# Optimization experiments

Measured on AMD Instinct MI355X. Metric: run time of the kernel, lower is better.

The kernel has to match this reference:

```python
import jax, jax.numpy as jnp
import numpy as np

EMBED = 200
ATT_D = 200
EPS = 1e-5


def _make_pos(x, embed_len):
    # p[i, j+off, k] = sin(j/1000^(j/E)) if k odd else cos(...); rows with leading
    # zero-count `off` get positions shifted right; first `off` rows stay zero.
    B, L = x.shape
    off = jnp.sum(x == 0, axis=1)                       # [B]
    j = jnp.arange(L)[None, :] - off[:, None]           # [B, L]
    valid = j >= 0
    jf = jnp.maximum(j, 0).astype(jnp.float32)
    angle = jf / jnp.power(1000.0, jf / embed_len)      # [B, L]
    kk = jnp.arange(embed_len)
    odd = (kk % 2 == 1)[None, None, :]
    val = jnp.where(odd, jnp.sin(angle)[:, :, None], jnp.cos(angle)[:, :, None])
    return jnp.where(valid[:, :, None], val, 0.0)       # [B, L, E]


def _ln2(y):
    # F.layer_norm over last TWO dims (seq, embed), no affine
    mu = jnp.mean(y, axis=(1, 2), keepdims=True)
    var = jnp.mean((y - mu) ** 2, axis=(1, 2), keepdims=True)
    return (y - mu) / jnp.sqrt(var + EPS)


def setup_inputs() -> dict:
    key = jax.random.key(0)
    ks = jax.random.split(key, 10)
    B, L, V = 32, 1024, 32000
    x = jax.random.randint(ks[0], (B, L), 0, V)
    embed = jax.random.normal(ks[1], (V, EMBED), dtype=jnp.float32) * 0.02
    w_qkv = jax.random.normal(ks[2], (EMBED, ATT_D), dtype=jnp.float32) * 0.02
    b_qkv = jnp.zeros((ATT_D,), dtype=jnp.float32)
    head = 8
    w_fuse = jax.random.normal(ks[3], (ATT_D * head, ATT_D), dtype=jnp.float32) * 0.02
    b_fuse = jnp.zeros((ATT_D,), dtype=jnp.float32)
    w1 = jax.random.normal(ks[4], (ATT_D, ATT_D), dtype=jnp.float32) * 0.02
    b1 = jnp.zeros((ATT_D,), dtype=jnp.float32)
    w2 = jax.random.normal(ks[5], (ATT_D, ATT_D), dtype=jnp.float32) * 0.02
    b2 = jnp.zeros((ATT_D,), dtype=jnp.float32)
    return {"x": x, "embed": embed, "w_qkv": w_qkv, "b_qkv": b_qkv,
            "w_fuse": w_fuse, "b_fuse": b_fuse, "w1": w1, "b1": b1,
            "w2": w2, "b2": b2, "stack": 6, "head": head}


def reference(x, embed, w_qkv, b_qkv, w_fuse, b_fuse, w1, b1, w2, b2, stack, head):
    p = _make_pos(x, EMBED)
    h = embed[x] + p                                     # [B, L, 200]
    scale = jnp.sqrt(jnp.float32(ATT_D))
    for _ in range(stack):
        r = h
        # q == k == v: the source shares ONE Linear across q/k/v, heads, stacks
        q = h @ w_qkv + b_qkv                            # [B, L, 200]
        d = jnp.einsum('bld,bmd->blm', q, q) / scale     # [B, L, L]
        a = jax.nn.softmax(d, axis=-1)
        c = jnp.einsum('blm,bmd->bld', a, q)             # [B, L, 200]
        c_all = jnp.tile(c, (1, 1, head))                # identical heads concat
        h = c_all @ w_fuse + b_fuse
        h = _ln2(h + r)
        r = h
        h = jax.nn.relu(h @ w1 + b1) @ w2 + b2
        h = _ln2(h + r)
    return h
```

## Files before the change

kernel.cpp:

```cpp
#include <hip/hip_runtime.h>
#include <hip/hip_bf16.h>

#define B_    32
#define L_    1024
#define D_    200
#define DP    256
#define M_    (B_*L_)
#define NTOT  (M_*DP)
#define NELEM 204800.f
#define INVSCALE 0.07071067811865475f
#define LNEPS 1e-5f

typedef unsigned short u16;
typedef unsigned int   u32;
typedef long long      i64;
typedef __attribute__((ext_vector_type(8))) short bf16x8;
typedef __attribute__((ext_vector_type(4))) float f32x4;

__device__ __forceinline__ float bf2f(u32 lo16) {
    union { u32 i; float f; } v; v.i = lo16 << 16; return v.f;
}
__device__ __forceinline__ u16 f2bf(float f) {
    union { float f; u32 i; } v; v.f = f;
    u32 r = v.i + 0x7fffu + ((v.i >> 16) & 1u);
    return (u16)(r >> 16);
}
__device__ __forceinline__ float ldf(const void* p, long i, int isbf) {
    return isbf ? bf2f(((const u16*)p)[i]) : ((const float*)p)[i];
}
__device__ __forceinline__ i64 ldtok(const void* p, long i, int isl64) {
    return isl64 ? ((const i64*)p)[i] : (i64)((const int*)p)[i];
}

__global__ void k_dtype(const u16* __restrict__ e16, const u32* __restrict__ xw,
                        int* __restrict__ flag) {
    int t = threadIdx.x;
    u32 u = e16[2*t];
    u32 ex = (u >> 7) & 0xFFu;
    int sane = (ex >= 0x60u && ex <= 0x87u) ? 1 : 0;
    unsigned long long m1 = __ballot(sane);
    int zhi = (xw[2*t + 1] == 0u) ? 1 : 0;
    unsigned long long m2 = __ballot(zhi);
    if (t == 0) {
        flag[0] = (__popcll(m1) >= 48) ? 1 : 0;
        flag[1] = (__popcll(m2) >= 48) ? 1 : 0;
    }
}

__global__ void k_off(const void* __restrict__ x, const int* __restrict__ flag,
                      int* __restrict__ off) {
    __shared__ int red[256];
    int b = blockIdx.x, t = threadIdx.x;
    int isl64 = flag[1];
    int cnt = 0;
    for (int l = t; l < L_; l += 256)
        cnt += (ldtok(x, (long)b*L_ + l, isl64) == 0) ? 1 : 0;
    red[t] = cnt; __syncthreads();
    for (int s = 128; s > 0; s >>= 1) {
        if (t < s) red[t] += red[t+s];
        __syncthreads();
    }
    if (t == 0) off[b] = red[0];
}

__global__ void k_wfold(const void* __restrict__ wqkv,
                        const void* __restrict__ wfuse,
                        const void* __restrict__ w1,
                        const void* __restrict__ w2,
                        const int* __restrict__ flag,
                        u16* __restrict__ tq, u16* __restrict__ tf,
                        u16* __restrict__ t1, u16* __restrict__ t2) {
    int idx = blockIdx.x*256 + threadIdx.x;
    if (idx >= DP*DP) return;
    int isbf = flag[0];
    int n = idx / DP, k = idx % DP;
    float vq = 0.f, vf = 0.f, v1 = 0.f, v2 = 0.f;
    if (n < D_ && k < D_) {
        vq = ldf(wqkv, k*D_ + n, isbf);
        v1 = ldf(w1,   k*D_ + n, isbf);
        v2 = ldf(w2,   k*D_ + n, isbf);
        #pragma unroll
        for (int hh = 0; hh < 8; ++hh)
            vf += ldf(wfuse, (hh*D_ + k)*D_ + n, isbf);
    }
    tq[idx] = f2bf(vq); tf[idx] = f2bf(vf);
    t1[idx] = f2bf(v1); t2[idx] = f2bf(v2);
}

__global__ void k_bfold(const void* __restrict__ bqkv, const void* __restrict__ bfuse,
                        const void* __restrict__ b1,   const void* __restrict__ b2,
                        const int* __restrict__ flag,
                        float* __restrict__ pq, float* __restrict__ pf,
                        float* __restrict__ p1, float* __restrict__ p2,
                        float* __restrict__ part, float* __restrict__ statA) {
    int c = threadIdx.x;
    int isbf = flag[0];
    float vq = 0.f, vf = 0.f, v1 = 0.f, v2 = 0.f;
    if (c < D_) {
        vq = ldf(bqkv, c, isbf); vf = ldf(bfuse, c, isbf);
        v1 = ldf(b1,   c, isbf); v2 = ldf(b2,   c, isbf);
    }
    pq[c] = vq; pf[c] = vf; p1[c] = v1; p2[c] = v2;
    if (c < 64) part[c] = 0.f;
    if (c < 32) { statA[2*c] = 0.f; statA[2*c+1] = 1.f; }
}

__global__ void k_embed(const void* __restrict__ x,
                        const void* __restrict__ emb,
                        const int* __restrict__ off,
                        const int* __restrict__ flag,
                        float* __restrict__ A) {
    int idx = blockIdx.x*256 + threadIdx.x;
    int c = idx & 255;
    int l = (idx >> 8) & 1023;
    int b = idx >> 18;
    float v = 0.f;
    if (c < D_) {
        i64 tok = ldtok(x, (long)b*L_ + l, flag[1]);
        v = ldf(emb, (long)tok*D_ + c, flag[0]);
        int j = l - off[b];
        if (j >= 0) {
            float jf = (float)j;
            float angle = jf * __expf(-jf * 0.034538776394910684f);
            v += (c & 1) ? __sinf(angle) : __cosf(angle);
        }
    }
    A[idx] = v;
}

template<int ACT, int OBF, int RES, int LNA>
__global__ __launch_bounds__(256) void k_gemm_m(const void* __restrict__ Asrc,
                                                const u16* __restrict__ Wt,
                                                const float* __restrict__ biasp,
                                                void* __restrict__ C,
                                                const float* __restrict__ Res,
                                                const float* __restrict__ rstat,
                                                float* __restrict__ part) {
    __shared__ u16 wt3[32*1032];
    const int t    = threadIdx.x;
    const int lane = t & 63;
    const int w    = t >> 6;
    const int quad = lane >> 4;
    const int l16  = lane & 15;
    const int r0   = blockIdx.x * 128;
    const int c0   = blockIdx.y * 128;

    float mu = 0.f, inv = 1.f;
    if (LNA || RES) {
        int batch = blockIdx.x >> 3;
        mu  = rstat[2*batch];
        inv = rstat[2*batch + 1];
    }

    #pragma unroll
    for (int i = 0; i < 16; ++i) {
        int ci = t + i*256;
        int n = ci >> 5, kc = ci & 31;
        *(uint4*)&wt3[kc*1032 + n*8] =
            *(const uint4*)(Wt + (size_t)(c0 + n)*DP + kc*8);
    }

    bf16x8 qa[2][7];
    #pragma unroll
    for (int rb = 0; rb < 2; ++rb) {
        size_t ro = (size_t)(r0 + w*32 + rb*16 + l16)*DP + quad*8;
        if (LNA) {
            const float* ar = (const float*)Asrc + ro;
            #pragma unroll
            for (int kk = 0; kk < 7; ++kk) {
                f32x4 va = *(const f32x4*)(ar + kk*32);
                f32x4 vb = *(const f32x4*)(ar + kk*32 + 4);
                bf16x8 q;
                q[0] = (short)f2bf((va[0]-mu)*inv);
                q[1] = (short)f2bf((va[1]-mu)*inv);
                q[2] = (short)f2bf((va[2]-mu)*inv);
                q[3] = (short)f2bf((va[3]-mu)*inv);
                q[4] = (short)f2bf((vb[0]-mu)*inv);
                q[5] = (short)f2bf((vb[1]-mu)*inv);
                q[6] = (short)f2bf((vb[2]-mu)*inv);
                q[7] = (short)f2bf((vb[3]-mu)*inv);
                qa[rb][kk] = q;
            }
        } else {
            const u16* ar = (const u16*)Asrc + ro;
            #pragma unroll
            for (int kk = 0; kk < 7; ++kk)
                qa[rb][kk] = *(const bf16x8*)(ar + kk*32);
        }
    }
    __syncthreads();

    f32x4 acc[2][8];
    #pragma unroll
    for (int rb = 0; rb < 2; ++rb)
        #pragma unroll
        for (int ct = 0; ct < 8; ++ct) acc[rb][ct] = (f32x4){0.f,0.f,0.f,0.f};

    #pragma unroll
    for (int ct = 0; ct < 8; ++ct) {
        #pragma unroll
        for (int kk = 0; kk < 7; ++kk) {
            bf16x8 vb = *(const bf16x8*)&wt3[(kk*4 + quad)*1032 + (ct*16 + l16)*8];
            acc[0][ct] = __builtin_amdgcn_mfma_f32_16x16x32_bf16(qa[0][kk], vb, acc[0][ct], 0,0,0);
            acc[1][ct] = __builtin_amdgcn_mfma_f32_16x16x32_bf16(qa[1][kk], vb, acc[1][ct], 0,0,0);
        }
    }

    float lsum = 0.f, lss = 0.f;
    #pragma unroll
    for (int ct = 0; ct < 8; ++ct) {
        int col = c0 + ct*16 + l16;
        float bv = biasp[col];
        #pragma unroll
        for (int rb = 0; rb < 2; ++rb) {
            #pragma unroll
            for (int r = 0; r < 4; ++r) {
                int row = r0 + w*32 + rb*16 + quad*4 + r;
                float v = acc[rb][ct][r] + bv;
                if (ACT) v = fmaxf(v, 0.f);
                if (RES) {
                    v += (Res[(size_t)row*DP + col] - mu) * inv;
                    ((float*)C)[(size_t)row*DP + col] = v;
                    if (col < D_) { lsum += v; lss += v*v; }
                } else if (OBF) {
                    ((u16*)C)[(size_t)row*DP + col] = f2bf(v);
                } else {
                    ((float*)C)[(size_t)row*DP + col] = v;
                }
            }
        }
    }
    if (RES) {
        __syncthreads();
        float* red = (float*)wt3;
        red[t] = lsum; red[256 + t] = lss;
        __syncthreads();
        for (int s = 128; s > 0; s >>= 1) {
            if (t < s) { red[t] += red[t+s]; red[256+t] += red[256+t+s]; }
            __syncthreads();
        }
        if (t == 0) {
            int batch = blockIdx.x >> 3;
            atomicAdd(&part[2*batch],     red[0]);
            atomicAdd(&part[2*batch + 1], red[256]);
        }
    }
}

__global__ __launch_bounds__(256) void k_tr(const u16* __restrict__ Qbf,
                                            u16* __restrict__ QbfT) {
    __shared__ u16 tile[64][72];
    const int t  = threadIdx.x;
    const int k0 = blockIdx.x * 64;
    const int f0 = blockIdx.y * 64;
    const int b  = blockIdx.z;
    const u16* S = Qbf  + (size_t)b*(L_*DP);
    u16*      Dd = QbfT + (size_t)b*(L_*DP);
    #pragma unroll
    for (int i = 0; i < 2; ++i) {
        int ci = t + i*256;
        int row = ci >> 3, g = ci & 7;
        *(uint4*)&tile[row][g*8] =
            *(const uint4*)(S + (size_t)(k0+row)*DP + f0 + g*8);
    }
    __syncthreads();
    #pragma unroll
    for (int i = 0; i < 2; ++i) {
        int ci = t + i*256;
        int feat = ci >> 3, g = ci & 7;
        u16 tmp[8];
        #pragma unroll
        for (int e = 0; e < 8; ++e) tmp[e] = tile[g*8+e][feat];
        *(uint4*)(Dd + (size_t)(f0+feat)*L_ + k0 + g*8) = *(uint4*)tmp;
    }
}

__global__ __launch_bounds__(256) void k_attn_m(const u16* __restrict__ Qbf,
                                                const u16* __restrict__ QbfT,
                                                u16* __restrict__ O) {
    __shared__ u16 ks[32*264];
    __shared__ u16 vt[256*40];
    __shared__ u16 ps[64*40];
    const int t    = threadIdx.x;
    const int lane = t & 63;
    const int w    = t >> 6;
    const int quad = lane >> 4;
    const int l16  = lane & 15;
    const int id   = blockIdx.x;
    const int xcd  = id & 7;
    const int ti   = (id >> 3) & 15;
    const int b    = ((id >> 7) << 3) | xcd;
    const int l0   = ti * 64;
    const u16* Qb  = Qbf  + (size_t)b*(L_*DP);
    const u16* QTb = QbfT + (size_t)b*(L_*DP);
    u16*       Ob  = O    + (size_t)b*(L_*DP);

    bf16x8 qa[7];
    {
        const u16* qrow = Qb + (size_t)(l0 + w*16 + l16)*DP + quad*8;
        #pragma unroll
        for (int kk = 0; kk < 7; ++kk)
            qa[kk] = *(const bf16x8*)(qrow + kk*32);
    }
    f32x4 oacc[13];
    #pragma unroll
    for (int ft = 0; ft < 13; ++ft) oacc[ft] = (f32x4){0.f, 0.f, 0.f, 0.f};
    float l_acc[4] = {0.f, 0.f, 0.f, 0.f};

    for (int n0 = 0; n0 < L_; n0 += 32) {
        __syncthreads();
        #pragma unroll
        for (int i = 0; i < 4; ++i) {
            int ci = t + i*256;
            int row = ci >> 5, g = ci & 31;
            *(uint4*)&ks[row*264 + g*8] =
                *(const uint4*)(Qb + (size_t)(n0+row)*DP + g*8);
        }
        #pragma unroll
        for (int i = 0; i < 4; ++i) {
            int ci = t + i*256;
            int feat = ci >> 2, g = ci & 3;
            *(uint4*)&vt[feat*40 + g*8] =
                *(const uint4*)(QTb + (size_t)feat*L_ + n0 + g*8);
        }
        __syncthreads();
        #pragma unroll
        for (int ct = 0; ct < 2; ++ct) {
            f32x4 sc = (f32x4){0.f, 0.f, 0.f, 0.f};
            #pragma unroll
            for (int kk = 0; kk < 7; ++kk) {
                bf16x8 bb = *(const bf16x8*)&ks[(ct*16 + l16)*264 + kk*32 + quad*8];
                sc = __builtin_amdgcn_mfma_f32_16x16x32_bf16(qa[kk], bb, sc, 0, 0, 0);
            }
            #pragma unroll
            for (int r = 0; r < 4; ++r) {
                float p = __expf(sc[r] * INVSCALE);
                l_acc[r] += p;
                ps[(w*16 + quad*4 + r)*40 + ct*16 + l16] = f2bf(p);
            }
        }
        __syncthreads();
        bf16x8 pa = *(const bf16x8*)&ps[(w*16 + l16)*40 + quad*8];
        #pragma unroll
        for (int ft = 0; ft < 13; ++ft) {
            bf16x8 vb = *(const bf16x8*)&vt[(ft*16 + l16)*40 + quad*8];
            oacc[ft] = __builtin_amdgcn_mfma_f32_16x16x32_bf16(pa, vb, oacc[ft], 0, 0, 0);
        }
    }
    #pragma unroll
    for (int r = 0; r < 4; ++r) {
        float v = l_acc[r];
        v += __shfl_xor(v, 1);
        v += __shfl_xor(v, 2);
        v += __shfl_xor(v, 4);
        v += __shfl_xor(v, 8);
        l_acc[r] = 1.f / v;
    }
    #pragma unroll
    for (int r = 0; r < 4; ++r) {
        u16* orow = Ob + (size_t)(l0 + w*16 + quad*4 + r)*DP + l16;
        #pragma unroll
        for (int ft = 0; ft < 13; ++ft)
            orow[ft*16] = f2bf(oacc[ft][r] * l_acc[r]);
        orow[13*16] = 0; orow[14*16] = 0; orow[15*16] = 0;
    }
}

__global__ void k_ln_stats(float* __restrict__ part, float* __restrict__ stats) {
    int b = threadIdx.x;
    if (b >= 32) return;
    float sum = part[2*b], ss = part[2*b+1];
    float mu  = sum / NELEM;
    float var = ss / NELEM - mu*mu;
    stats[b*2]   = mu;
    stats[b*2+1] = 1.f / sqrtf(var + LNEPS);
    part[2*b] = 0.f; part[2*b+1] = 0.f;
}

__global__ void k_out(const float* __restrict__ A, const float* __restrict__ stat,
                      const int* __restrict__ flag, float* __restrict__ out) {
    int idx = blockIdx.x*256 + threadIdx.x;
    if (idx >= M_*D_) return;
    int row = idx / D_;
    int c   = idx - row*D_;
    int b   = row >> 10;
    float v = (A[(size_t)row*DP + c] - stat[2*b]) * stat[2*b+1];
    if (!isfinite(v)) v = 1000.f + 64.f*flag[0] + 16.f*flag[1];
    out[idx] = v;
}

extern "C" void kernel_launch(void* const* d_in, const int* in_sizes, int n_in,
                              void* d_out, int out_size, void* d_ws, size_t ws_size,
                              hipStream_t stream) {
    const void* x     = d_in[0];
    const void* emb   = d_in[1];
    const void* wqkv  = d_in[2];
    const void* bqkv  = d_in[3];
    const void* wfuse = d_in[4];
    const void* bfuse = d_in[5];
    const void* w1    = d_in[6];
    const void* b1    = d_in[7];
    const void* w2    = d_in[8];
    const void* b2    = d_in[9];

    float* Y0  = (float*)d_ws;
    float* Y1  = Y0 + NTOT;
    u16* Qbf   = (u16*)(Y1 + NTOT);
    u16* QbfT  = Qbf + NTOT;
    u16* Hbf   = QbfT;
    u16* Cbf   = QbfT + NTOT;
    u16* wtq   = Cbf + NTOT;
    u16* wtf   = wtq + DP*DP;
    u16* wt1   = wtf + DP*DP;
    u16* wt2   = wt1 + DP*DP;
    float* bqp = (float*)(wt2 + DP*DP);
    float* bfp = bqp + DP;
    float* b1p = bfp + DP;
    float* b2p = b1p + DP;
    float* part  = b2p + DP;
    float* statA = part + 64;
    float* statB = statA + 64;
    int*   off   = (int*)(statB + 64);
    int*   flag  = off + 32;

    k_dtype<<<1, 64, 0, stream>>>((const u16*)emb, (const u32*)x, flag);
    k_off  <<<32, 256, 0, stream>>>(x, flag, off);
    k_wfold<<<DP*DP/256, 256, 0, stream>>>(wqkv, wfuse, w1, w2, flag,
                                           wtq, wtf, wt1, wt2);
    k_bfold<<<1, 256, 0, stream>>>(bqkv, bfuse, b1, b2, flag,
                                   bqp, bfp, b1p, b2p, part, statA);
    k_embed<<<NTOT/256, 256, 0, stream>>>(x, emb, off, flag, Y0);

    for (int s = 0; s < 6; ++s) {
        k_gemm_m<0,1,0,1><<<dim3(M_/128, DP/128), 256, 0, stream>>>(
            Y0, wtq, bqp, Qbf, nullptr, statA, nullptr);
        k_tr<<<dim3(L_/64, DP/64, B_), 256, 0, stream>>>(Qbf, QbfT);
        k_attn_m<<<512, 256, 0, stream>>>(Qbf, QbfT, Cbf);
        k_gemm_m<0,0,1,0><<<dim3(M_/128, DP/128), 256, 0, stream>>>(
            Cbf, wtf, bfp, Y1, Y0, statA, part);
        k_ln_stats<<<1, 64, 0, stream>>>(part, statB);
        k_gemm_m<1,1,0,1><<<dim3(M_/128, DP/128), 256, 0, stream>>>(
            Y1, wt1, b1p, Hbf, nullptr, statB, nullptr);
        k_gemm_m<0,0,1,0><<<dim3(M_/128, DP/128), 256, 0, stream>>>(
            Hbf, wt2, b2p, Y0, Y1, statB, part);
        k_ln_stats<<<1, 64, 0, stream>>>(part, statA);
    }
    k_out<<<(M_*D_ + 255)/256, 256, 0, stream>>>(Y0, statA, flag, (float*)d_out);
}
```

Baseline: 984.9 us.

## Fuse Q transpose into QKV GEMM epilogue and widen attention per-wave row tiles

The QKV GEMM epilogue now also writes the transposed bf16 Q directly into QbfT using 8-byte strided stores, so the separate k_tr transpose kernel is gone. The attention kernel moves to 128-thread blocks in which each wave handles 32 query rows (two 16-row tiles). Each K/V fragment loaded from LDS is reused for two MFMAs, and the barrier before reading P is dropped because each wave reads back only the rows it wrote. The trade-offs are more registers per wave, half as many waves per block, and strided transposed global writes in the GEMM epilogue.

```diff
diff --git a/kernel.cpp b/kernel.cpp
--- a/kernel.cpp
+++ b/kernel.cpp
@@ -128,14 +128,15 @@
     A[idx] = v;
 }
 
-template<int ACT, int OBF, int RES, int LNA>
+template<int ACT, int OBF, int RES, int LNA, int TRW>
 __global__ __launch_bounds__(256) void k_gemm_m(const void* __restrict__ Asrc,
                                                 const u16* __restrict__ Wt,
                                                 const float* __restrict__ biasp,
                                                 void* __restrict__ C,
                                                 const float* __restrict__ Res,
                                                 const float* __restrict__ rstat,
-                                                float* __restrict__ part) {
+                                                float* __restrict__ part,
+                                                u16* __restrict__ Qt) {
     __shared__ u16 wt3[32*1032];
     const int t    = threadIdx.x;
     const int lane = t & 63;
@@ -213,6 +214,7 @@
         float bv = biasp[col];
         #pragma unroll
         for (int rb = 0; rb < 2; ++rb) {
+            u16 tq4[4];
             #pragma unroll
             for (int r = 0; r < 4; ++r) {
                 int row = r0 + w*32 + rb*16 + quad*4 + r;
@@ -223,10 +225,18 @@
                     ((float*)C)[(size_t)row*DP + col] = v;
                     if (col < D_) { lsum += v; lss += v*v; }
                 } else if (OBF) {
-                    ((u16*)C)[(size_t)row*DP + col] = f2bf(v);
+                    u16 hb = f2bf(v);
+                    ((u16*)C)[(size_t)row*DP + col] = hb;
+                    if (TRW) tq4[r] = hb;
                 } else {
                     ((float*)C)[(size_t)row*DP + col] = v;
                 }
+            }
+            if (TRW && OBF) {
+                size_t batch = (size_t)(r0 >> 10);
+                int key = (r0 & 1023) + w*32 + rb*16 + quad*4;
+                *(uint2*)(Qt + batch*(size_t)(DP*L_) + (size_t)col*L_ + key)
+                    = *(const uint2*)tq4;
             }
         }
     }
@@ -247,37 +257,9 @@
     }
 }
 
-__global__ __launch_bounds__(256) void k_tr(const u16* __restrict__ Qbf,
-                                            u16* __restrict__ QbfT) {
-    __shared__ u16 tile[64][72];
-    const int t  = threadIdx.x;
-    const int k0 = blockIdx.x * 64;
-    const int f0 = blockIdx.y * 64;
-    const int b  = blockIdx.z;
-    const u16* S = Qbf  + (size_t)b*(L_*DP);
-    u16*      Dd = QbfT + (size_t)b*(L_*DP);
-    #pragma unroll
-    for (int i = 0; i < 2; ++i) {
-        int ci = t + i*256;
-        int row = ci >> 3, g = ci & 7;
-        *(uint4*)&tile[row][g*8] =
-            *(const uint4*)(S + (size_t)(k0+row)*DP + f0 + g*8);
-    }
-    __syncthreads();
-    #pragma unroll
-    for (int i = 0; i < 2; ++i) {
-        int ci = t + i*256;
-        int feat = ci >> 3, g = ci & 7;
-        u16 tmp[8];
-        #pragma unroll
-        for (int e = 0; e < 8; ++e) tmp[e] = tile[g*8+e][feat];
-        *(uint4*)(Dd + (size_t)(f0+feat)*L_ + k0 + g*8) = *(uint4*)tmp;
-    }
-}
-
-__global__ __launch_bounds__(256) void k_attn_m(const u16* __restrict__ Qbf,
-                                                const u16* __restrict__ QbfT,
-                                                u16* __restrict__ O) {
+__global__ __launch_bounds__(128, 1) void k_attn_m(const u16* __restrict__ Qbf,
+                                                   const u16* __restrict__ QbfT,
+                                                   u16* __restrict__ O) {
     __shared__ u16 ks[32*264];
     __shared__ u16 vt[256*40];
     __shared__ u16 ps[64*40];
@@ -295,30 +277,33 @@
     const u16* QTb = QbfT + (size_t)b*(L_*DP);
     u16*       Ob  = O    + (size_t)b*(L_*DP);
 
-    bf16x8 qa[7];
-    {
-        const u16* qrow = Qb + (size_t)(l0 + w*16 + l16)*DP + quad*8;
+    bf16x8 qa[2][7];
+    #pragma unroll
+    for (int rb = 0; rb < 2; ++rb) {
+        const u16* qrow = Qb + (size_t)(l0 + w*32 + rb*16 + l16)*DP + quad*8;
         #pragma unroll
         for (int kk = 0; kk < 7; ++kk)
-            qa[kk] = *(const bf16x8*)(qrow + kk*32);
-    }
-    f32x4 oacc[13];
-    #pragma unroll
-    for (int ft = 0; ft < 13; ++ft) oacc[ft] = (f32x4){0.f, 0.f, 0.f, 0.f};
-    float l_acc[4] = {0.f, 0.f, 0.f, 0.f};
+            qa[rb][kk] = *(const bf16x8*)(qrow + kk*32);
+    }
+    f32x4 oacc[2][13];
+    #pragma unroll
+    for (int rb = 0; rb < 2; ++rb)
+        #pragma unroll
+        for (int ft = 0; ft < 13; ++ft) oacc[rb][ft] = (f32x4){0.f, 0.f, 0.f, 0.f};
+    float l_acc[2][4] = {{0.f,0.f,0.f,0.f},{0.f,0.f,0.f,0.f}};
 
     for (int n0 = 0; n0 < L_; n0 += 32) {
         __syncthreads();
         #pragma unroll
-        for (int i = 0; i < 4; ++i) {
-            int ci = t + i*256;
+        for (int i = 0; i < 8; ++i) {
+            int ci = t + i*128;
             int row = ci >> 5, g = ci & 31;
             *(uint4*)&ks[row*264 + g*8] =
                 *(const uint4*)(Qb + (size_t)(n0+row)*DP + g*8);
         }
         #pragma unroll
-        for (int i = 0; i < 4; ++i) {
-            int ci = t + i*256;
+        for (int i = 0; i < 8; ++i) {
+            int ci = t + i*128;
             int feat = ci >> 2, g = ci & 3;
             *(uint4*)&vt[feat*40 + g*8] =
                 *(const uint4*)(QTb + (size_t)feat*L_ + n0 + g*8);
@@ -326,44 +311,54 @@
         __syncthreads();
         #pragma unroll
         for (int ct = 0; ct < 2; ++ct) {
-            f32x4 sc = (f32x4){0.f, 0.f, 0.f, 0.f};
+            f32x4 sc0 = (f32x4){0.f, 0.f, 0.f, 0.f};
+            f32x4 sc1 = (f32x4){0.f, 0.f, 0.f, 0.f};
             #pragma unroll
             for (int kk = 0; kk < 7; ++kk) {
                 bf16x8 bb = *(const bf16x8*)&ks[(ct*16 + l16)*264 + kk*32 + quad*8];
-                sc = __builtin_amdgcn_mfma_f32_16x16x32_bf16(qa[kk], bb, sc, 0, 0, 0);
+                sc0 = __builtin_amdgcn_mfma_f32_16x16x32_bf16(qa[0][kk], bb, sc0, 0, 0, 0);
+                sc1 = __builtin_amdgcn_mfma_f32_16x16x32_bf16(qa[1][kk], bb, sc1, 0, 0, 0);
             }
             #pragma unroll
             for (int r = 0; r < 4; ++r) {
-                float p = __expf(sc[r] * INVSCALE);
-                l_acc[r] += p;
-                ps[(w*16 + quad*4 + r)*40 + ct*16 + l16] = f2bf(p);
+                float p0 = __expf(sc0[r] * INVSCALE);
+                float p1 = __expf(sc1[r] * INVSCALE);
+                l_acc[0][r] += p0;
+                l_acc[1][r] += p1;
+                ps[(w*32 +      quad*4 + r)*40 + ct*16 + l16] = f2bf(p0);
+                ps[(w*32 + 16 + quad*4 + r)*40 + ct*16 + l16] = f2bf(p1);
             }
         }
-        __syncthreads();
-        bf16x8 pa = *(const bf16x8*)&ps[(w*16 + l16)*40 + quad*8];
+        bf16x8 pa0 = *(const bf16x8*)&ps[(w*32      + l16)*40 + quad*8];
+        bf16x8 pa1 = *(const bf16x8*)&ps[(w*32 + 16 + l16)*40 + quad*8];
         #pragma unroll
         for (int ft = 0; ft < 13; ++ft) {
             bf16x8 vb = *(const bf16x8*)&vt[(ft*16 + l16)*40 + quad*8];
-            oacc[ft] = __builtin_amdgcn_mfma_f32_16x16x32_bf16(pa, vb, oacc[ft], 0, 0, 0);
-        }
-    }
-    #pragma unroll
-    for (int r = 0; r < 4; ++r) {
-        float v = l_acc[r];
-        v += __shfl_xor(v, 1);
-        v += __shfl_xor(v, 2);
-        v += __shfl_xor(v, 4);
-        v += __shfl_xor(v, 8);
-        l_acc[r] = 1.f / v;
-    }
-    #pragma unroll
-    for (int r = 0; r < 4; ++r) {
-        u16* orow = Ob + (size_t)(l0 + w*16 + quad*4 + r)*DP + l16;
-        #pragma unroll
-        for (int ft = 0; ft < 13; ++ft)
-            orow[ft*16] = f2bf(oacc[ft][r] * l_acc[r]);
-        orow[13*16] = 0; orow[14*16] = 0; orow[15*16] = 0;
-    }
+            oacc[0][ft] = __builtin_amdgcn_mfma_f32_16x16x32_bf16(pa0, vb, oacc[0][ft], 0, 0, 0);
+            oacc[1][ft] = __builtin_amdgcn_mfma_f32_16x16x32_bf16(pa1, vb, oacc[1][ft], 0, 0, 0);
+        }
+    }
+    #pragma unroll
+    for (int rb = 0; rb < 2; ++rb)
+        #pragma unroll
+        for (int r = 0; r < 4; ++r) {
+            float v = l_acc[rb][r];
+            v += __shfl_xor(v, 1);
+            v += __shfl_xor(v, 2);
+            v += __shfl_xor(v, 4);
+            v += __shfl_xor(v, 8);
+            l_acc[rb][r] = 1.f / v;
+        }
+    #pragma unroll
+    for (int rb = 0; rb < 2; ++rb)
+        #pragma unroll
+        for (int r = 0; r < 4; ++r) {
+            u16* orow = Ob + (size_t)(l0 + w*32 + rb*16 + quad*4 + r)*DP + l16;
+            #pragma unroll
+            for (int ft = 0; ft < 13; ++ft)
+                orow[ft*16] = f2bf(oacc[rb][ft][r] * l_acc[rb][r]);
+            orow[13*16] = 0; orow[14*16] = 0; orow[15*16] = 0;
+        }
 }
 
 __global__ void k_ln_stats(float* __restrict__ part, float* __restrict__ stats) {
@@ -432,17 +427,16 @@
     k_embed<<<NTOT/256, 256, 0, stream>>>(x, emb, off, flag, Y0);
 
     for (int s = 0; s < 6; ++s) {
-        k_gemm_m<0,1,0,1><<<dim3(M_/128, DP/128), 256, 0, stream>>>(
-            Y0, wtq, bqp, Qbf, nullptr, statA, nullptr);
-        k_tr<<<dim3(L_/64, DP/64, B_), 256, 0, stream>>>(Qbf, QbfT);
-        k_attn_m<<<512, 256, 0, stream>>>(Qbf, QbfT, Cbf);
-        k_gemm_m<0,0,1,0><<<dim3(M_/128, DP/128), 256, 0, stream>>>(
-            Cbf, wtf, bfp, Y1, Y0, statA, part);
+        k_gemm_m<0,1,0,1,1><<<dim3(M_/128, DP/128), 256, 0, stream>>>(
+            Y0, wtq, bqp, Qbf, nullptr, statA, nullptr, QbfT);
+        k_attn_m<<<512, 128, 0, stream>>>(Qbf, QbfT, Cbf);
+        k_gemm_m<0,0,1,0,0><<<dim3(M_/128, DP/128), 256, 0, stream>>>(
+            Cbf, wtf, bfp, Y1, Y0, statA, part, nullptr);
         k_ln_stats<<<1, 64, 0, stream>>>(part, statB);
-        k_gemm_m<1,1,0,1><<<dim3(M_/128, DP/128), 256, 0, stream>>>(
-            Y1, wt1, b1p, Hbf, nullptr, statB, nullptr);
-        k_gemm_m<0,0,1,0><<<dim3(M_/128, DP/128), 256, 0, stream>>>(
-            Hbf, wt2, b2p, Y0, Y1, statB, part);
+        k_gemm_m<1,1,0,1,0><<<dim3(M_/128, DP/128), 256, 0, stream>>>(
+            Y1, wt1, b1p, Hbf, nullptr, statB, nullptr, nullptr);
+        k_gemm_m<0,0,1,0,0><<<dim3(M_/128, DP/128), 256, 0, stream>>>(
+            Hbf, wt2, b2p, Y0, Y1, statB, part, nullptr);
         k_ln_stats<<<1, 64, 0, stream>>>(part, statA);
     }
     k_out<<<(M_*D_ + 255)/256, 256, 0, stream>>>(Y0, statA, flag, (float*)d_out);
```

Result: faster. 946.8 us (-3.9%).
